# Kernel tuning notes

Measured on AMD Instinct MI355X. Metric: run time of the kernel, lower is better.

The kernel has to match this reference:

```python
import jax, jax.numpy as jnp
import numpy as np

WS = 7           # window_size
NUM_HEADS = 4
DIM = 128
BNW = 4096       # batch * num_windows
NW = 64          # windows per image (attn_mask leading dim)
N = WS * WS      # tokens per window = 49


def make_rel_idx(ws: int) -> np.ndarray:
    coords = np.stack(np.meshgrid(np.arange(ws), np.arange(ws), indexing='ij'))  # (2, ws, ws)
    flat = coords.reshape(2, -1)                                                  # (2, N)
    rel = flat[:, :, None] - flat[:, None, :]                                     # (2, N, N)
    rel = rel.transpose(1, 2, 0).copy()
    rel[:, :, 0] += ws - 1
    rel[:, :, 1] += ws - 1
    rel[:, :, 0] *= 2 * ws - 1
    return rel.sum(-1).astype(np.int32)                                           # (N, N)


def setup_inputs() -> dict:
    key = jax.random.key(0)
    ks = jax.random.split(key, 4)
    x = jax.random.normal(ks[0], (BNW, N, DIM), dtype=jnp.float32)
    attn_mask = jnp.zeros((NW, N, N), dtype=jnp.float32)
    qkv_w = jax.random.normal(ks[1], (3 * DIM, DIM), dtype=jnp.float32) * 0.02
    qkv_b = jnp.zeros((3 * DIM,), dtype=jnp.float32)
    proj_w = jax.random.normal(ks[2], (DIM, DIM), dtype=jnp.float32) * 0.02
    proj_b = jnp.zeros((DIM,), dtype=jnp.float32)
    bias_table = jax.random.normal(ks[3], ((2 * WS - 1) ** 2, NUM_HEADS), dtype=jnp.float32) * 0.02
    rel_idx = jnp.asarray(make_rel_idx(WS))
    return {"x": x, "attn_mask": attn_mask, "qkv_w": qkv_w, "qkv_b": qkv_b,
            "proj_w": proj_w, "proj_b": proj_b, "bias_table": bias_table,
            "rel_idx": rel_idx}


def reference(x, attn_mask, qkv_w, qkv_b, proj_w, proj_b, bias_table, rel_idx):
    BnW, n, C = x.shape
    H = NUM_HEADS
    hd = C // H
    scale = hd ** -0.5
    # qkv projection: (BnW, n, 3C) -> (3, BnW, H, n, hd)
    qkv = (x @ qkv_w.T + qkv_b).reshape(BnW, n, 3, H, hd).transpose(2, 0, 3, 1, 4)
    q, k, v = qkv[0], qkv[1], qkv[2]
    attn = jnp.einsum('bhnd,bhmd->bhnm', q * scale, k)          # (BnW, H, n, n)
    bias = bias_table[rel_idx]                                   # (n, n, H)
    attn = attn + bias.transpose(2, 0, 1)[None]                  # broadcast (1, H, n, n)
    nW = attn_mask.shape[0]
    attn = attn.reshape(-1, nW, H, n, n) + attn_mask[None, :, None]
    attn = attn.reshape(-1, H, n, n)
    attn = jax.nn.softmax(attn, axis=-1)
    out = jnp.einsum('bhnm,bhmd->bhnd', attn, v)                 # (BnW, H, n, hd)
    out = out.transpose(0, 2, 1, 3).reshape(BnW, n, C)
    return out @ proj_w.T + proj_b
```

## Files before the change

### kernel.cpp

```cpp
#include <hip/hip_runtime.h>

#define NT   49
#define HD   32
#define NH   4
#define DIM  128
#define SCALEQ 0.17677669529663687f

typedef __attribute__((ext_vector_type(8))) short short8;
typedef __attribute__((ext_vector_type(4))) short short4v;
typedef __attribute__((ext_vector_type(4))) float floatx4;
typedef short8 short8a __attribute__((may_alias));
typedef short4v short4a __attribute__((may_alias));
typedef unsigned long long ulla __attribute__((may_alias));
typedef unsigned long long ull;

__device__ __forceinline__ short f2b(float f) {
    union { float f; unsigned u; } v; v.f = f;
    return (short)((v.u + 0x7fffu + ((v.u >> 16) & 1u)) >> 16);
}
__device__ __forceinline__ float b2f(short s) {
    union { unsigned u; float f; } v; v.u = ((unsigned)(unsigned short)s) << 16;
    return v.f;
}

__global__ void wmsa_prep(const float* __restrict__ qkvw, const float* __restrict__ projw,
                          const float* __restrict__ btab, const int* __restrict__ ridx,
                          short* __restrict__ wqkv, short* __restrict__ wproj,
                          short* __restrict__ b4) {
    int i = blockIdx.x * 256 + threadIdx.x;
    if (i < 3 * DIM * DIM) {
        float s = (i < DIM * DIM) ? SCALEQ : 1.0f;
        wqkv[i] = f2b(qkvw[i] * s);
    }
    if (i < DIM * DIM) wproj[i] = f2b(projw[i]);
    if (i < NH * 64 * 64) {
        int h = i >> 12, row = (i >> 6) & 63, col = i & 63;
        float v;
        if (col >= NT)      v = -1e30f;
        else if (row >= NT) v = 0.f;
        else                v = btab[ridx[row * NT + col] * NH + h];
        int it = row >> 4, qq = (row >> 2) & 3, r = row & 3;
        int jt = col >> 4, cc = col & 15;
        b4[(((h * 4 + it) * 4 + jt) * 4 + qq) * 64 + cc * 4 + r] = f2b(v);
    }
}

#define RWAVE 12800
#define OSTR  136
#define LDSB  51200

__global__ __launch_bounds__(256, 3) void wmsa_main(
    const float* __restrict__ x, const float* __restrict__ mask,
    const float* __restrict__ qkvb, const float* __restrict__ projb,
    const short* __restrict__ wqkv, const short* __restrict__ wproj,
    const short* __restrict__ b4, float* __restrict__ out)
{
    __shared__ __align__(16) char pool[LDSB];
    short* lds = (short*)pool;

    const int b    = blockIdx.x;
    const int wdw  = b & 63;
    const int tid  = threadIdx.x;
    const int wave = tid >> 6;
    const int lane = tid & 63;
    const int qq   = lane >> 4;
    const int cc   = lane & 15;
    const int ccl  = cc & 7, cch = cc >> 3, cm3 = cc & 3;

    {
        const float* xb = x + (size_t)b * NT * DIM;
        for (int i = tid; i < NT * 32; i += 256) {
            int t = i >> 5, c4 = (i & 31) << 2;
            float4 v = *(const float4*)(xb + t * DIM + c4);
            ull pk =  (ull)(unsigned short)f2b(v.x)
                    | ((ull)(unsigned short)f2b(v.y) << 16)
                    | ((ull)(unsigned short)f2b(v.z) << 32)
                    | ((ull)(unsigned short)f2b(v.w) << 48);
            *(ulla*)(lds + t * 136 + c4) = pk;
        }
        for (int i = tid; i < (64 - NT) * 32; i += 256) {
            int t = NT + (i >> 5), c4 = (i & 31) << 2;
            *(ulla*)(lds + t * 136 + c4) = 0ull;
        }
    }
    __syncthreads();

    short8 af[4][4];
    #pragma unroll
    for (int it = 0; it < 4; ++it)
        #pragma unroll
        for (int ks = 0; ks < 4; ++ks)
            af[it][ks] = *(const short8a*)(lds + (it * 16 + cc) * 136 + ks * 32 + qq * 8);
    __syncthreads();

    short* qw = (short*)(pool + wave * RWAVE);
    short* kw = qw + 2048;
    short* vw = qw + 4096;
    short* pw = qw;

    #pragma unroll
    for (int jt6 = 0; jt6 < 6; ++jt6) {
        const int sec = jt6 >> 1, hlf = jt6 & 1;
        const int col = sec * DIM + wave * 32 + hlf * 16 + cc;
        short8 bf[4];
        #pragma unroll
        for (int ks = 0; ks < 4; ++ks)
            bf[ks] = *(const short8a*)(wqkv + col * DIM + ks * 32 + qq * 8);
        float bias = qkvb[col];
        if (sec == 0) bias *= SCALEQ;
        const floatx4 cinit = {bias, bias, bias, bias};
        #pragma unroll
        for (int it = 0; it < 4; ++it) {
            floatx4 acc = cinit;
            #pragma unroll
            for (int ks = 0; ks < 4; ++ks)
                acc = __builtin_amdgcn_mfma_f32_16x16x32_bf16(af[it][ks], bf[ks], acc, 0, 0, 0);
            if (sec == 2) {
                int dd = hlf * 16 + cc;
                int t0 = it * 16 + qq * 4;
                ull pk =  (ull)(unsigned short)f2b(acc[0])
                        | ((ull)(unsigned short)f2b(acc[1]) << 16)
                        | ((ull)(unsigned short)f2b(acc[2]) << 32)
                        | ((ull)(unsigned short)f2b(acc[3]) << 48);
                *(ulla*)(vw + dd * 72 + t0) = pk;
            } else {
                short* dst = (sec == 0) ? qw : kw;
                int gb = hlf * 2 + cch;
                #pragma unroll
                for (int r = 0; r < 4; ++r) {
                    int t = it * 16 + qq * 4 + r;
                    dst[t * 32 + ((gb ^ r) << 3) + ccl] = f2b(acc[r]);
                }
            }
        }
    }
    __asm__ volatile("" ::: "memory");

    {
        short8 qf[4], kf[4];
        #pragma unroll
        for (int t = 0; t < 4; ++t) {
            qf[t] = *(const short8a*)(qw + (t * 16 + cc) * 32 + ((qq ^ cm3) << 3));
            kf[t] = *(const short8a*)(kw + (t * 16 + cc) * 32 + ((qq ^ cm3) << 3));
        }
        const short* b4w = b4 + wave * 4096;
        const float* mw  = mask + (size_t)wdw * NT * NT;
        #pragma unroll
        for (int it = 0; it < 4; ++it) {
            floatx4 s[4];
            #pragma unroll
            for (int jt = 0; jt < 4; ++jt) {
                short4v cb = *(const short4a*)(b4w + ((it * 4 + jt) * 4 + qq) * 64 + cc * 4);
                floatx4 ci = {b2f(cb.x), b2f(cb.y), b2f(cb.z), b2f(cb.w)};
                s[jt] = __builtin_amdgcn_mfma_f32_16x16x32_bf16(qf[it], kf[jt], ci, 0, 0, 0);
            }
            float e[4][4], inv[4];
            #pragma unroll
            for (int r = 0; r < 4; ++r) {
                int row = it * 16 + qq * 4 + r;
                float sm = 0.f;
                #pragma unroll
                for (int jt = 0; jt < 4; ++jt) {
                    int colj = jt * 16 + cc;
                    float mv = (row < NT && colj < NT) ? mw[row * NT + colj] : 0.f;
                    float ee = __expf(s[jt][r] + mv);
                    e[r][jt] = ee;
                    sm += ee;
                }
                #pragma unroll
                for (int d = 1; d < 16; d <<= 1) sm += __shfl_xor(sm, d);
                inv[r] = 1.0f / sm;
            }
            #pragma unroll
            for (int r = 0; r < 4; ++r) {
                int t = it * 16 + qq * 4 + r;
                #pragma unroll
                for (int jt = 0; jt < 4; ++jt) {
                    int g = (jt * 2 + cch) ^ r;
                    pw[t * 64 + (g << 3) + ccl] = f2b(e[r][jt] * inv[r]);
                }
            }
        }
    }
    __asm__ volatile("" ::: "memory");

    floatx4 o[4][2];
    #pragma unroll
    for (int it = 0; it < 4; ++it)
        #pragma unroll
        for (int jv = 0; jv < 2; ++jv)
            o[it][jv] = (floatx4){0.f, 0.f, 0.f, 0.f};
    #pragma unroll
    for (int ks = 0; ks < 2; ++ks) {
        short8 pf[4], vf[2];
        #pragma unroll
        for (int it = 0; it < 4; ++it)
            pf[it] = *(const short8a*)(pw + (it * 16 + cc) * 64 + (((ks * 4 + qq) ^ cm3) << 3));
        #pragma unroll
        for (int jv = 0; jv < 2; ++jv)
            vf[jv] = *(const short8a*)(vw + (jv * 16 + cc) * 72 + ks * 32 + qq * 8);
        #pragma unroll
        for (int it = 0; it < 4; ++it)
            #pragma unroll
            for (int jv = 0; jv < 2; ++jv)
                o[it][jv] = __builtin_amdgcn_mfma_f32_16x16x32_bf16(pf[it], vf[jv], o[it][jv], 0, 0, 0);
    }
    __syncthreads();

    short* ow = (short*)pool;
    #pragma unroll
    for (int it = 0; it < 4; ++it)
        #pragma unroll
        for (int jv = 0; jv < 2; ++jv)
            #pragma unroll
            for (int r = 0; r < 4; ++r) {
                int t = it * 16 + qq * 4 + r;
                ow[t * OSTR + wave * 32 + jv * 16 + cc] = f2b(o[it][jv][r]);
            }
    __syncthreads();

    {
        short8 a2[4];
        #pragma unroll
        for (int ks = 0; ks < 4; ++ks)
            a2[ks] = *(const short8a*)(ow + (wave * 16 + cc) * OSTR + ks * 32 + qq * 8);
        float* outb = out + (size_t)b * NT * DIM;
        #pragma unroll
        for (int jt = 0; jt < 8; ++jt) {
            int col = jt * 16 + cc;
            short8 bfp[4];
            #pragma unroll
            for (int ks = 0; ks < 4; ++ks)
                bfp[ks] = *(const short8a*)(wproj + col * DIM + ks * 32 + qq * 8);
            float pb = projb[col];
            floatx4 acc = {pb, pb, pb, pb};
            #pragma unroll
            for (int ks = 0; ks < 4; ++ks)
                acc = __builtin_amdgcn_mfma_f32_16x16x32_bf16(a2[ks], bfp[ks], acc, 0, 0, 0);
            #pragma unroll
            for (int r = 0; r < 4; ++r) {
                int row = wave * 16 + qq * 4 + r;
                if (row < NT) outb[row * DIM + col] = acc[r];
            }
        }
    }
}

extern "C" void kernel_launch(void* const* d_in, const int* in_sizes, int n_in,
                              void* d_out, int out_size, void* d_ws, size_t ws_size,
                              hipStream_t stream) {
    const float* x     = (const float*)d_in[0];
    const float* mask  = (const float*)d_in[1];
    const float* qkvw  = (const float*)d_in[2];
    const float* qkvb  = (const float*)d_in[3];
    const float* projw = (const float*)d_in[4];
    const float* projb = (const float*)d_in[5];
    const float* btab  = (const float*)d_in[6];
    const int*   ridx  = (const int*)d_in[7];
    float* outp = (float*)d_out;

    short* wqkv  = (short*)d_ws;
    short* wproj = (short*)((char*)d_ws + 98304);
    short* b4    = (short*)((char*)d_ws + 131072);

    wmsa_prep<<<192, 256, 0, stream>>>(qkvw, projw, btab, ridx, wqkv, wproj, b4);
    wmsa_main<<<4096, 256, 0, stream>>>(x, mask, qkvb, projb, wqkv, wproj, b4, outp);
}
```

Baseline: 325.9 us.

## Fold attention mask into precomputed bf16 bias table and prefetch weight fragments

The prep kernel now builds a per-window combined relative-position-bias plus attention-mask table in bf16, already laid out in MFMA fragment order. The main kernel loads it as one short4 per tile instead of doing scattered fp32 mask reads with bounds checks inside the softmax. QKV and projection weight fragments are software-prefetched one or two tiles ahead, and biases are hoisted. The cost is a larger prep launch and extra workspace, the mask is rounded to bf16, and register pressure rises.

```diff
diff --git a/kernel.cpp b/kernel.cpp
--- a/kernel.cpp
+++ b/kernel.cpp
@@ -25,23 +25,28 @@
 
 __global__ void wmsa_prep(const float* __restrict__ qkvw, const float* __restrict__ projw,
                           const float* __restrict__ btab, const int* __restrict__ ridx,
+                          const float* __restrict__ mask,
                           short* __restrict__ wqkv, short* __restrict__ wproj,
-                          short* __restrict__ b4) {
+                          short* __restrict__ cmb) {
     int i = blockIdx.x * 256 + threadIdx.x;
     if (i < 3 * DIM * DIM) {
         float s = (i < DIM * DIM) ? SCALEQ : 1.0f;
         wqkv[i] = f2b(qkvw[i] * s);
     }
     if (i < DIM * DIM) wproj[i] = f2b(projw[i]);
-    if (i < NH * 64 * 64) {
-        int h = i >> 12, row = (i >> 6) & 63, col = i & 63;
+    if (i < 64 * NH * 4096) {
+        int wdw = i >> 14, rem = i & 16383;
+        int h = rem >> 12, e = rem & 4095;
+        int tile = e >> 8, r2 = e & 255;
+        int it = tile >> 2, jt = tile & 3;
+        int qq = r2 >> 6, cr = r2 & 63, cc = cr >> 2, r = cr & 3;
+        int row = it * 16 + qq * 4 + r, col = jt * 16 + cc;
         float v;
         if (col >= NT)      v = -1e30f;
         else if (row >= NT) v = 0.f;
-        else                v = btab[ridx[row * NT + col] * NH + h];
-        int it = row >> 4, qq = (row >> 2) & 3, r = row & 3;
-        int jt = col >> 4, cc = col & 15;
-        b4[(((h * 4 + it) * 4 + jt) * 4 + qq) * 64 + cc * 4 + r] = f2b(v);
+        else                v = btab[ridx[row * NT + col] * NH + h]
+                              + mask[wdw * NT * NT + row * NT + col];
+        cmb[i] = f2b(v);
     }
 }
 
@@ -50,10 +55,10 @@
 #define LDSB  51200
 
 __global__ __launch_bounds__(256, 3) void wmsa_main(
-    const float* __restrict__ x, const float* __restrict__ mask,
+    const float* __restrict__ x,
     const float* __restrict__ qkvb, const float* __restrict__ projb,
     const short* __restrict__ wqkv, const short* __restrict__ wproj,
-    const short* __restrict__ b4, float* __restrict__ out)
+    const short* __restrict__ cmb, float* __restrict__ out)
 {
     __shared__ __align__(16) char pool[LDSB];
     short* lds = (short*)pool;
@@ -66,6 +71,16 @@
     const int qq   = lane >> 4;
     const int cc   = lane & 15;
     const int ccl  = cc & 7, cch = cc >> 3, cm3 = cc & 3;
+
+    const int colbase = wave * 32 + cc;
+    short8 bfc[4], bfn[4];
+    #pragma unroll
+    for (int ks = 0; ks < 4; ++ks)
+        bfc[ks] = *(const short8a*)(wqkv + colbase * DIM + ks * 32 + qq * 8);
+    float biasv[6];
+    #pragma unroll
+    for (int j = 0; j < 6; ++j)
+        biasv[j] = qkvb[(j >> 1) * DIM + colbase + (j & 1) * 16];
 
     {
         const float* xb = x + (size_t)b * NT * DIM;
@@ -101,12 +116,13 @@
     #pragma unroll
     for (int jt6 = 0; jt6 < 6; ++jt6) {
         const int sec = jt6 >> 1, hlf = jt6 & 1;
-        const int col = sec * DIM + wave * 32 + hlf * 16 + cc;
-        short8 bf[4];
-        #pragma unroll
-        for (int ks = 0; ks < 4; ++ks)
-            bf[ks] = *(const short8a*)(wqkv + col * DIM + ks * 32 + qq * 8);
-        float bias = qkvb[col];
+        if (jt6 < 5) {
+            const int cn = ((jt6 + 1) >> 1) * DIM + colbase + ((jt6 + 1) & 1) * 16;
+            #pragma unroll
+            for (int ks = 0; ks < 4; ++ks)
+                bfn[ks] = *(const short8a*)(wqkv + cn * DIM + ks * 32 + qq * 8);
+        }
+        float bias = biasv[jt6];
         if (sec == 0) bias *= SCALEQ;
         const floatx4 cinit = {bias, bias, bias, bias};
         #pragma unroll
@@ -114,7 +130,7 @@
             floatx4 acc = cinit;
             #pragma unroll
             for (int ks = 0; ks < 4; ++ks)
-                acc = __builtin_amdgcn_mfma_f32_16x16x32_bf16(af[it][ks], bf[ks], acc, 0, 0, 0);
+                acc = __builtin_amdgcn_mfma_f32_16x16x32_bf16(af[it][ks], bfc[ks], acc, 0, 0, 0);
             if (sec == 2) {
                 int dd = hlf * 16 + cc;
                 int t0 = it * 16 + qq * 4;
@@ -133,6 +149,16 @@
                 }
             }
         }
+        #pragma unroll
+        for (int ks = 0; ks < 4; ++ks) bfc[ks] = bfn[ks];
+    }
+
+    short4v cm[16];
+    {
+        const short* cw = cmb + (((size_t)wdw * NH + wave) << 12);
+        #pragma unroll
+        for (int t16 = 0; t16 < 16; ++t16)
+            cm[t16] = *(const short4a*)(cw + t16 * 256 + qq * 64 + cc * 4);
     }
     __asm__ volatile("" ::: "memory");
 
@@ -143,27 +169,22 @@
             qf[t] = *(const short8a*)(qw + (t * 16 + cc) * 32 + ((qq ^ cm3) << 3));
             kf[t] = *(const short8a*)(kw + (t * 16 + cc) * 32 + ((qq ^ cm3) << 3));
         }
-        const short* b4w = b4 + wave * 4096;
-        const float* mw  = mask + (size_t)wdw * NT * NT;
         #pragma unroll
         for (int it = 0; it < 4; ++it) {
             floatx4 s[4];
             #pragma unroll
             for (int jt = 0; jt < 4; ++jt) {
-                short4v cb = *(const short4a*)(b4w + ((it * 4 + jt) * 4 + qq) * 64 + cc * 4);
+                short4v cb = cm[it * 4 + jt];
                 floatx4 ci = {b2f(cb.x), b2f(cb.y), b2f(cb.z), b2f(cb.w)};
                 s[jt] = __builtin_amdgcn_mfma_f32_16x16x32_bf16(qf[it], kf[jt], ci, 0, 0, 0);
             }
             float e[4][4], inv[4];
             #pragma unroll
             for (int r = 0; r < 4; ++r) {
-                int row = it * 16 + qq * 4 + r;
                 float sm = 0.f;
                 #pragma unroll
                 for (int jt = 0; jt < 4; ++jt) {
-                    int colj = jt * 16 + cc;
-                    float mv = (row < NT && colj < NT) ? mw[row * NT + colj] : 0.f;
-                    float ee = __expf(s[jt][r] + mv);
+                    float ee = __expf(s[jt][r]);
                     e[r][jt] = ee;
                     sm += ee;
                 }
@@ -205,6 +226,17 @@
             for (int jv = 0; jv < 2; ++jv)
                 o[it][jv] = __builtin_amdgcn_mfma_f32_16x16x32_bf16(pf[it], vf[jv], o[it][jv], 0, 0, 0);
     }
+
+    short8 pcur[4], pnxt[4];
+    float pbv[8];
+    #pragma unroll
+    for (int ks = 0; ks < 4; ++ks) {
+        pcur[ks] = *(const short8a*)(wproj + cc * DIM + ks * 32 + qq * 8);
+        pnxt[ks] = *(const short8a*)(wproj + (16 + cc) * DIM + ks * 32 + qq * 8);
+    }
+    #pragma unroll
+    for (int j = 0; j < 8; ++j) pbv[j] = projb[j * 16 + cc];
+
     __syncthreads();
 
     short* ow = (short*)pool;
@@ -227,21 +259,26 @@
         float* outb = out + (size_t)b * NT * DIM;
         #pragma unroll
         for (int jt = 0; jt < 8; ++jt) {
+            short8 pfut[4];
+            if (jt < 6) {
+                int cn = (jt + 2) * 16 + cc;
+                #pragma unroll
+                for (int ks = 0; ks < 4; ++ks)
+                    pfut[ks] = *(const short8a*)(wproj + cn * DIM + ks * 32 + qq * 8);
+            }
+            float pb = pbv[jt];
+            floatx4 acc = {pb, pb, pb, pb};
+            #pragma unroll
+            for (int ks = 0; ks < 4; ++ks)
+                acc = __builtin_amdgcn_mfma_f32_16x16x32_bf16(a2[ks], pcur[ks], acc, 0, 0, 0);
             int col = jt * 16 + cc;
-            short8 bfp[4];
-            #pragma unroll
-            for (int ks = 0; ks < 4; ++ks)
-                bfp[ks] = *(const short8a*)(wproj + col * DIM + ks * 32 + qq * 8);
-            float pb = projb[col];
-            floatx4 acc = {pb, pb, pb, pb};
-            #pragma unroll
-            for (int ks = 0; ks < 4; ++ks)
-                acc = __builtin_amdgcn_mfma_f32_16x16x32_bf16(a2[ks], bfp[ks], acc, 0, 0, 0);
             #pragma unroll
             for (int r = 0; r < 4; ++r) {
                 int row = wave * 16 + qq * 4 + r;
                 if (row < NT) outb[row * DIM + col] = acc[r];
             }
+            #pragma unroll
+            for (int ks = 0; ks < 4; ++ks) { pcur[ks] = pnxt[ks]; pnxt[ks] = pfut[ks]; }
         }
     }
 }
@@ -261,8 +298,8 @@
 
     short* wqkv  = (short*)d_ws;
     short* wproj = (short*)((char*)d_ws + 98304);
-    short* b4    = (short*)((char*)d_ws + 131072);
-
-    wmsa_prep<<<192, 256, 0, stream>>>(qkvw, projw, btab, ridx, wqkv, wproj, b4);
-    wmsa_main<<<4096, 256, 0, stream>>>(x, mask, qkvb, projb, wqkv, wproj, b4, outp);
-}
+    short* cmb   = (short*)((char*)d_ws + 131072);
+
+    wmsa_prep<<<4096, 256, 0, stream>>>(qkvw, projw, btab, ridx, mask, wqkv, wproj, cmb);
+    wmsa_main<<<4096, 256, 0, stream>>>(x, qkvb, projb, wqkv, wproj, cmb, outp);
+}
```

Result: faster. 301.6 us (-7.5%).
